# Optimization experiments

Hardware: AMD Instinct MI355X
Metric: run time of the kernel (lower is better)

The kernel has to match this reference:

```python
import jax, jax.numpy as jnp
import numpy as np

N_NODES = 100000
N_EDGES = 1600000
F_IN = 128
HID = 128
N_LAYERS = 4
N_CLASSES = 10
N_GRAPHS = 512
BN_EPS = 1e-5


def setup_inputs() -> dict:
    key = jax.random.key(0)
    ks = jax.random.split(key, 16)
    x = jax.random.normal(ks[0], (N_NODES, F_IN), dtype=jnp.float32)
    edge_index = jax.random.randint(ks[1], (2, N_EDGES), 0, N_NODES, dtype=jnp.int64)
    edge_attr = jax.random.normal(ks[2], (N_EDGES, 8), dtype=jnp.float32)
    batch = jnp.sort(jax.random.randint(ks[3], (N_NODES,), 0, N_GRAPHS, dtype=jnp.int64))
    # Per-layer MLP params (in-dim is 128 for all layers since F_IN == HID).
    s1 = 1.0 / np.sqrt(F_IN)
    s2 = 1.0 / np.sqrt(2 * HID)
    W1 = jax.random.uniform(ks[4], (N_LAYERS, F_IN, 2 * HID), minval=-s1, maxval=s1, dtype=jnp.float32)
    b1 = jax.random.uniform(ks[5], (N_LAYERS, 2 * HID), minval=-s1, maxval=s1, dtype=jnp.float32)
    gamma1 = jnp.ones((N_LAYERS, 2 * HID), dtype=jnp.float32)
    beta1 = jnp.zeros((N_LAYERS, 2 * HID), dtype=jnp.float32)
    W2 = jax.random.uniform(ks[6], (N_LAYERS, 2 * HID, HID), minval=-s2, maxval=s2, dtype=jnp.float32)
    b2 = jax.random.uniform(ks[7], (N_LAYERS, HID), minval=-s2, maxval=s2, dtype=jnp.float32)
    sf = 1.0 / np.sqrt(HID * N_LAYERS)
    fcW = jax.random.uniform(ks[8], (HID * N_LAYERS, N_CLASSES), minval=-sf, maxval=sf, dtype=jnp.float32)
    fcb = jax.random.uniform(ks[9], (N_CLASSES,), minval=-sf, maxval=sf, dtype=jnp.float32)
    return {"x": x, "edge_index": edge_index, "edge_attr": edge_attr, "batch": batch,
            "W1": W1, "b1": b1, "gamma1": gamma1, "beta1": beta1,
            "W2": W2, "b2": b2, "fcW": fcW, "fcb": fcb}


def reference(x, edge_index, edge_attr, batch, W1, b1, gamma1, beta1, W2, b2, fcW, fcb):
    # edge_attr is unused by the original forward.
    src, dst = edge_index[0], edge_index[1]
    n = x.shape[0]
    # In-degree for mean aggregation (messages flow src -> dst in PyG).
    deg = jax.ops.segment_sum(jnp.ones((src.shape[0],), x.dtype), dst, num_segments=n)
    inv_deg = 1.0 / jnp.maximum(deg, 1.0)
    h = x
    xs = []
    for i in range(N_LAYERS):
        # GINConv, eps=0, aggr='mean': nn(x + mean_j h_j)
        agg = jax.ops.segment_sum(h[src], dst, num_segments=n) * inv_deg[:, None]
        z = h + agg
        z = z @ W1[i] + b1[i]                      # [N, 2H]
        mu = jnp.mean(z, axis=0)
        var = jnp.mean(jnp.square(z - mu), axis=0)  # biased var (BN training mode)
        z = gamma1[i] * (z - mu) * jax.lax.rsqrt(var + BN_EPS) + beta1[i]
        z = jax.nn.relu(z)
        z = z @ W2[i] + b2[i]                      # [N, H]
        h = jax.nn.relu(z)
        xs.append(h)
    xcat = jnp.concatenate(xs, axis=1)             # [N, H*L]
    # global_mean_pool over graph ids
    gsum = jax.ops.segment_sum(xcat, batch, num_segments=N_GRAPHS)
    gcnt = jax.ops.segment_sum(jnp.ones((n,), xcat.dtype), batch, num_segments=N_GRAPHS)
    pooled = gsum / jnp.maximum(gcnt, 1.0)[:, None]
    logits = pooled @ fcW + fcb
    return jax.nn.log_softmax(logits, axis=-1)
```

## Files before the change

kernel.cpp:

```cpp
#include <hip/hip_runtime.h>
#include <cstdint>
#include <cstddef>

#define NN 100000
#define NE 1600000
#define FD 128
#define HD2 256
#define NLAYERS 4
#define NGR 512
#define NCLS 10
#define BNEPS 1e-5f
#define G1TILES 1563
#define GEMM_GRID 512
#define MLP_GRID 256
#define EB 6250
#define NB 391
#define NSLICE 8
#define SLICEW 12500

typedef unsigned short ushort_t;
typedef short bf16x8 __attribute__((ext_vector_type(8)));
typedef float f32x4 __attribute__((ext_vector_type(4)));

__device__ __forceinline__ float bfl(unsigned short u) {
  unsigned v = ((unsigned)u) << 16;
  return __builtin_bit_cast(float, v);
}
__device__ __forceinline__ unsigned short fbf(float f) {
  unsigned u = __builtin_bit_cast(unsigned, f);
  unsigned r = (u + 0x7FFFu + ((u >> 16) & 1u)) >> 16;
  return (unsigned short)r;
}

__global__ void k_init_detect(const int* ei, int* flag, int* degi) {
  int i = blockIdx.x * 256 + threadIdx.x;
  if (i < NN) degi[i] = 0;
  if (blockIdx.x == 0) {
    __shared__ int nz;
    if (threadIdx.x == 0) nz = 0;
    __syncthreads();
    if (ei[2 * threadIdx.x + 1] != 0) atomicAdd(&nz, 1);
    __syncthreads();
    if (threadIdx.x == 0) flag[0] = (nz == 0) ? 1 : 0;
  }
}

__global__ void k_repack(const int* ei, const int* batch, const int* flag,
                         int* src32, int* dst32, int* batch32) {
  int i = blockIdx.x * 256 + threadIdx.x;
  const bool wide = (flag[0] != 0);
  if (i < NE) {
    src32[i] = wide ? ei[2 * i] : ei[i];
    dst32[i] = wide ? ei[2 * (NE + i)] : ei[NE + i];
  }
  if (i < NN) batch32[i] = wide ? batch[2 * i] : batch[i];
}

__global__ void k_deg8(const int* __restrict__ dst, int* degi) {
  int slice = blockIdx.x & (NSLICE - 1);
  int e = (blockIdx.x >> 3) * 256 + threadIdx.x;
  if (e >= NE) return;
  int d = dst[e];
  int lo = slice * SLICEW;
  if (d >= lo && d < lo + SLICEW) atomicAdd(&degi[d], 1);
}

__global__ void k_scan1(const int* degi, int* rowptr, int* bsum) {
  __shared__ int s[256];
  int t = threadIdx.x;
  int i = blockIdx.x * 256 + t;
  int v = (i < NN) ? degi[i] : 0;
  s[t] = v;
  __syncthreads();
  for (int off = 1; off < 256; off <<= 1) {
    int x = (t >= off) ? s[t - off] : 0;
    __syncthreads();
    s[t] += x;
    __syncthreads();
  }
  if (i < NN) rowptr[i] = s[t] - v;
  if (t == 255) bsum[blockIdx.x] = s[255];
}

__global__ void k_scan2_gstats(int* bsum, int nb, const int* __restrict__ batch,
                               int* __restrict__ gstart, int* __restrict__ gcnti) {
  __shared__ int s[512];
  int t = threadIdx.x;
  int v = (t < nb) ? bsum[t] : 0;
  s[t] = v;
  __syncthreads();
  for (int off = 1; off < 512; off <<= 1) {
    int x = (t >= off) ? s[t - off] : 0;
    __syncthreads();
    s[t] += x;
    __syncthreads();
  }
  if (t < nb) bsum[t] = s[t] - v;
  if (t < NGR) {
    int g = t;
    int lo = 0, hi = NN;
    while (lo < hi) { int m = (lo + hi) >> 1; if (batch[m] < g) lo = m + 1; else hi = m; }
    int st = lo;
    hi = NN;
    while (lo < hi) { int m = (lo + hi) >> 1; if (batch[m] < g + 1) lo = m + 1; else hi = m; }
    gstart[g] = st;
    gcnti[g] = lo - st;
  }
}

__global__ void k_scan3_cursor(int* rowptr, const int* bsum, int* cursor,
                               const int* degi, float* inv_deg) {
  int i = blockIdx.x * 256 + threadIdx.x;
  if (i < NN) {
    int r = rowptr[i] + bsum[blockIdx.x];
    rowptr[i] = r;
    cursor[i] = r;
    inv_deg[i] = 1.f / fmaxf((float)degi[i], 1.f);
  }
  if (i == 0) rowptr[NN] = NE;
}

__global__ void k_scatter8(const int* __restrict__ src, const int* __restrict__ dst,
                           int* cursor, int* csr) {
  int slice = blockIdx.x & (NSLICE - 1);
  int e = (blockIdx.x >> 3) * 256 + threadIdx.x;
  if (e >= NE) return;
  int d = dst[e];
  int lo = slice * SLICEW;
  if (d >= lo && d < lo + SLICEW) {
    int p = atomicAdd(&cursor[d], 1);
    csr[p] = src[e];
  }
}

__global__ void k_cvt_x(const float* __restrict__ x, ushort_t* __restrict__ xb) {
  int i = blockIdx.x * 256 + threadIdx.x;
  if (i >= NN * FD / 8) return;
  const float4* p = (const float4*)x + (size_t)i * 2;
  float4 a = p[0], b = p[1];
  bf16x8 o;
  o[0] = (short)fbf(a.x); o[1] = (short)fbf(a.y);
  o[2] = (short)fbf(a.z); o[3] = (short)fbf(a.w);
  o[4] = (short)fbf(b.x); o[5] = (short)fbf(b.y);
  o[6] = (short)fbf(b.z); o[7] = (short)fbf(b.w);
  *(bf16x8*)&xb[(size_t)i * 8] = o;
}

__global__ void k_cvt_w(const float* __restrict__ W1, const float* __restrict__ W2,
                        ushort_t* __restrict__ W1t, ushort_t* __restrict__ W2t) {
  int idx = blockIdx.x * 256 + threadIdx.x;
  if (idx >= NLAYERS * FD * HD2) return;
  int l = idx >> 15, r = idx & 32767;
  {
    int n = r >> 7, k = r & 127;
    W1t[(size_t)l * 32768 + n * 128 + k] = fbf(W1[(size_t)l * 32768 + k * 256 + n]);
  }
  {
    int n = r >> 8, k = r & 255;
    W2t[(size_t)l * 32768 + n * 256 + k] = fbf(W2[(size_t)l * 32768 + k * 128 + n]);
  }
}

__global__ void k_agg(const ushort_t* __restrict__ h, const int* __restrict__ rowptr,
                      const int* __restrict__ csr, const float* __restrict__ inv_deg,
                      ushort_t* __restrict__ tout, float* bnsum) {
  if (blockIdx.x == 0) {
    bnsum[threadIdx.x] = 0.f;
    bnsum[HD2 + threadIdx.x] = 0.f;
  }
  const int wave = threadIdx.x >> 6;
  const int lane = threadIdx.x & 63;
  const int q = lane >> 4, sub = lane & 15;
  const int node = blockIdx.x * 16 + wave * 4 + q;
  const uint4* h16 = (const uint4*)h;
  int beg = rowptr[node];
  int deg = rowptr[node + 1] - beg;
  int m1 = max(deg, __shfl_xor(deg, 16));
  int maxd = max(m1, __shfl_xor(m1, 32));
  float a0 = 0.f, a1 = 0.f, a2 = 0.f, a3 = 0.f;
  float a4 = 0.f, a5 = 0.f, a6 = 0.f, a7 = 0.f;
  int j = 0;
  for (; j + 8 <= maxd; j += 8) {
    uint4 p[8];
#pragma unroll
    for (int u = 0; u < 8; ++u) {
      bool valid = (j + u) < deg;
      int idx = beg + (valid ? j + u : 0);
      int s = csr[idx];
      uint4 v = h16[(size_t)s * 16 + sub];
      p[u].x = valid ? v.x : 0u;
      p[u].y = valid ? v.y : 0u;
      p[u].z = valid ? v.z : 0u;
      p[u].w = valid ? v.w : 0u;
    }
#pragma unroll
    for (int u = 0; u < 8; ++u) {
      a0 += bfl((unsigned short)(p[u].x & 0xFFFF));
      a1 += bfl((unsigned short)(p[u].x >> 16));
      a2 += bfl((unsigned short)(p[u].y & 0xFFFF));
      a3 += bfl((unsigned short)(p[u].y >> 16));
      a4 += bfl((unsigned short)(p[u].z & 0xFFFF));
      a5 += bfl((unsigned short)(p[u].z >> 16));
      a6 += bfl((unsigned short)(p[u].w & 0xFFFF));
      a7 += bfl((unsigned short)(p[u].w >> 16));
    }
  }
  for (; j < maxd; ++j) {
    bool valid = j < deg;
    int idx = beg + (valid ? j : 0);
    int s = csr[idx];
    uint4 v = h16[(size_t)s * 16 + sub];
    if (valid) {
      a0 += bfl((unsigned short)(v.x & 0xFFFF));
      a1 += bfl((unsigned short)(v.x >> 16));
      a2 += bfl((unsigned short)(v.y & 0xFFFF));
      a3 += bfl((unsigned short)(v.y >> 16));
      a4 += bfl((unsigned short)(v.z & 0xFFFF));
      a5 += bfl((unsigned short)(v.z >> 16));
      a6 += bfl((unsigned short)(v.w & 0xFFFF));
      a7 += bfl((unsigned short)(v.w >> 16));
    }
  }
  float id = inv_deg[node];
  uint4 c = h16[(size_t)node * 16 + sub];
  float o0 = bfl((unsigned short)(c.x & 0xFFFF)) + a0 * id;
  float o1 = bfl((unsigned short)(c.x >> 16)) + a1 * id;
  float o2 = bfl((unsigned short)(c.y & 0xFFFF)) + a2 * id;
  float o3 = bfl((unsigned short)(c.y >> 16)) + a3 * id;
  float o4 = bfl((unsigned short)(c.z & 0xFFFF)) + a4 * id;
  float o5 = bfl((unsigned short)(c.z >> 16)) + a5 * id;
  float o6 = bfl((unsigned short)(c.w & 0xFFFF)) + a6 * id;
  float o7 = bfl((unsigned short)(c.w >> 16)) + a7 * id;
  uint4 ow;
  ow.x = (unsigned)fbf(o0) | ((unsigned)fbf(o1) << 16);
  ow.y = (unsigned)fbf(o2) | ((unsigned)fbf(o3) << 16);
  ow.z = (unsigned)fbf(o4) | ((unsigned)fbf(o5) << 16);
  ow.w = (unsigned)fbf(o6) | ((unsigned)fbf(o7) << 16);
  ((uint4*)tout)[(size_t)node * 16 + sub] = ow;
}

__launch_bounds__(256, 2)
__global__ void k_zstat(const ushort_t* __restrict__ A, const ushort_t* __restrict__ Bt,
                        const float* __restrict__ bias, float* __restrict__ bnsum) {
  __shared__ ushort_t Bs[256 * 128];
  __shared__ ushort_t As[64 * 128];
  const int tid = threadIdx.x;
#pragma unroll
  for (int i = 0; i < 16; ++i) {
    int chunk = tid + 256 * i;
    int n = chunk >> 4, c = chunk & 15;
    bf16x8 v = *(const bf16x8*)&Bt[n * 128 + c * 8];
    *(bf16x8*)((char*)Bs + n * 256 + ((c * 16) ^ ((n & 7) << 4))) = v;
  }
  const int wv = tid >> 6, ln = tid & 63;
  const int lr = ln & 15, lg = ln >> 4;
  float bb[16];
#pragma unroll
  for (int nt = 0; nt < 16; ++nt) bb[nt] = bias[nt * 16 + lr];
  float s0[16] = {}, s1[16] = {};

  for (int t = blockIdx.x; t < G1TILES; t += GEMM_GRID) {
    int row0 = t * 64;
#pragma unroll
    for (int i = 0; i < 4; ++i) {
      int chunk = tid + 256 * i;
      int r = chunk >> 4, c = chunk & 15;
      int grow = row0 + r; if (grow >= NN) grow = NN - 1;
      bf16x8 v = *(const bf16x8*)&A[(size_t)grow * FD + c * 8];
      *(bf16x8*)((char*)As + r * 256 + ((c * 16) ^ ((r & 7) << 4))) = v;
    }
    __syncthreads();
    int arow = wv * 16 + lr;
    bf16x8 af[4];
#pragma unroll
    for (int ks = 0; ks < 4; ++ks)
      af[ks] = *(bf16x8*)((char*)As + arow * 256 + ((ks * 64 + lg * 16) ^ ((arow & 7) << 4)));
    f32x4 acc[16];
#pragma unroll
    for (int nt = 0; nt < 16; ++nt) acc[nt] = (f32x4){0.f, 0.f, 0.f, 0.f};
#pragma unroll
    for (int nt = 0; nt < 16; ++nt) {
      int bn = nt * 16 + lr;
#pragma unroll
      for (int ks = 0; ks < 4; ++ks) {
        bf16x8 bfr = *(bf16x8*)((char*)Bs + bn * 256 + ((ks * 64 + lg * 16) ^ ((bn & 7) << 4)));
        acc[nt] = __builtin_amdgcn_mfma_f32_16x16x32_bf16(af[ks], bfr, acc[nt], 0, 0, 0);
      }
    }
    __syncthreads();
#pragma unroll
    for (int nt = 0; nt < 16; ++nt) {
#pragma unroll
      for (int j = 0; j < 4; ++j) {
        int grow = row0 + wv * 16 + lg * 4 + j;
        if (grow < NN) {
          float zf = acc[nt][j] + bb[nt];
          s0[nt] += zf;
          s1[nt] += zf * zf;
        }
      }
    }
  }
  __syncthreads();
  float* ls = (float*)As;
  ls[tid] = 0.f; ls[tid + 256] = 0.f;
  __syncthreads();
#pragma unroll
  for (int nt = 0; nt < 16; ++nt) {
    int col = nt * 16 + lr;
    atomicAdd(&ls[col], s0[nt]);
    atomicAdd(&ls[col + 256], s1[nt]);
  }
  __syncthreads();
  if (tid < 256) {
    atomicAdd(&bnsum[tid], ls[tid]);
    atomicAdd(&bnsum[HD2 + tid], ls[tid + 256]);
  }
}

__launch_bounds__(512, 2)
__global__ void k_mlp(const ushort_t* __restrict__ T, const ushort_t* __restrict__ W1t,
                      const ushort_t* __restrict__ W2t, const float* __restrict__ b1,
                      const float* __restrict__ b2, const float* __restrict__ bnsum,
                      const float* __restrict__ gamma, const float* __restrict__ beta,
                      ushort_t* __restrict__ Hout) {
  __shared__ ushort_t W1s[256 * 128];
  __shared__ ushort_t W2s[128 * 256];
  __shared__ ushort_t ZR[64 * 256];
  const int tid = threadIdx.x;
#pragma unroll
  for (int i = 0; i < 8; ++i) {
    int chunk = tid + 512 * i;
    int n = chunk >> 4, c = chunk & 15;
    bf16x8 v = *(const bf16x8*)&W1t[n * 128 + c * 8];
    *(bf16x8*)((char*)W1s + n * 256 + ((c * 16) ^ ((n & 7) << 4))) = v;
  }
#pragma unroll
  for (int i = 0; i < 8; ++i) {
    int chunk = tid + 512 * i;
    int n = chunk >> 5, c = chunk & 31;
    bf16x8 v = *(const bf16x8*)&W2t[n * 256 + c * 8];
    *(bf16x8*)((char*)W2s + n * 512 + ((c * 16) ^ ((n & 7) << 4))) = v;
  }
  const int wv = tid >> 6, ln = tid & 63;
  const int lr = ln & 15, lg = ln >> 4;
  const int mrow = (wv & 3) * 16;
  const int nh = wv >> 2;
  float a1v[8], a2v[8], bb1[8];
#pragma unroll
  for (int nt = 0; nt < 8; ++nt) {
    int c = (nh * 8 + nt) * 16 + lr;
    float mu = bnsum[c] * (1.f / (float)NN);
    float var = fmaxf(bnsum[HD2 + c] * (1.f / (float)NN) - mu * mu, 0.f);
    float g = gamma[c] * rsqrtf(var + BNEPS);
    a1v[nt] = g;
    a2v[nt] = beta[c] - mu * g;
    bb1[nt] = b1[c];
  }
  float bb2[4];
#pragma unroll
  for (int nt2 = 0; nt2 < 4; ++nt2) bb2[nt2] = b2[nh * 64 + nt2 * 16 + lr];
  __syncthreads();

  for (int t = blockIdx.x; t < G1TILES; t += MLP_GRID) {
    int row0 = t * 64;
    int grow = row0 + mrow + lr; if (grow >= NN) grow = NN - 1;
    bf16x8 af[4];
#pragma unroll
    for (int ks = 0; ks < 4; ++ks)
      af[ks] = *(const bf16x8*)&T[(size_t)grow * FD + ks * 32 + lg * 8];
    f32x4 acc1[8];
#pragma unroll
    for (int nt = 0; nt < 8; ++nt) acc1[nt] = (f32x4){0.f, 0.f, 0.f, 0.f};
#pragma unroll
    for (int nt = 0; nt < 8; ++nt) {
      int bn = (nh * 8 + nt) * 16 + lr;
#pragma unroll
      for (int ks = 0; ks < 4; ++ks) {
        bf16x8 bfr = *(bf16x8*)((char*)W1s + bn * 256 + ((ks * 64 + lg * 16) ^ ((bn & 7) << 4)));
        acc1[nt] = __builtin_amdgcn_mfma_f32_16x16x32_bf16(af[ks], bfr, acc1[nt], 0, 0, 0);
      }
    }
#pragma unroll
    for (int nt = 0; nt < 8; ++nt) {
      int col = (nh * 8 + nt) * 16 + lr;
#pragma unroll
      for (int j = 0; j < 4; ++j) {
        int row = mrow + lg * 4 + j;
        float z = acc1[nt][j] + bb1[nt];
        float f = fmaxf(z * a1v[nt] + a2v[nt], 0.f);
        int byte = row * 512 + ((((col >> 3) << 4) ^ ((row & 7) << 4))) + (col & 7) * 2;
        *(ushort_t*)((char*)ZR + byte) = fbf(f);
      }
    }
    __syncthreads();
    int zrow = mrow + lr;
    bf16x8 af2[8];
#pragma unroll
    for (int ks2 = 0; ks2 < 8; ++ks2) {
      int c2 = ks2 * 4 + lg;
      af2[ks2] = *(bf16x8*)((char*)ZR + zrow * 512 + ((c2 * 16) ^ ((zrow & 7) << 4)));
    }
    __syncthreads();
    f32x4 acc2[4];
#pragma unroll
    for (int nt2 = 0; nt2 < 4; ++nt2) acc2[nt2] = (f32x4){0.f, 0.f, 0.f, 0.f};
#pragma unroll
    for (int nt2 = 0; nt2 < 4; ++nt2) {
      int bn2 = nh * 64 + nt2 * 16 + lr;
#pragma unroll
      for (int ks2 = 0; ks2 < 8; ++ks2) {
        int c2 = ks2 * 4 + lg;
        bf16x8 bfr2 = *(bf16x8*)((char*)W2s + bn2 * 512 + ((c2 * 16) ^ ((bn2 & 7) << 4)));
        acc2[nt2] = __builtin_amdgcn_mfma_f32_16x16x32_bf16(af2[ks2], bfr2, acc2[nt2], 0, 0, 0);
      }
    }
#pragma unroll
    for (int nt2 = 0; nt2 < 4; ++nt2) {
      int col = nh * 64 + nt2 * 16 + lr;
#pragma unroll
      for (int j = 0; j < 4; ++j) {
        int hrow = row0 + mrow + lg * 4 + j;
        if (hrow < NN) Hout[(size_t)hrow * FD + col] = fbf(fmaxf(acc2[nt2][j] + bb2[nt2], 0.f));
      }
    }
  }
}

__launch_bounds__(256)
__global__ void k_pool_fc(const ushort_t* __restrict__ hb, const int* __restrict__ gstart,
                          const int* __restrict__ gcnti, const float* __restrict__ fcW,
                          const float* __restrict__ fcb, float* __restrict__ out) {
  __shared__ float pool4[4][512];
  __shared__ float wred[4][NCLS];
  int g = blockIdx.x, t = threadIdx.x;
  int start = gstart[g], cnt = gcnti[g];
  int chunk = t & 63, ro = t >> 6;
  int L = chunk >> 4, cc = (chunk & 15) * 8;
  const ushort_t* hL = hb + (size_t)L * NN * FD;
  float s[8] = {};
  for (int r = start + ro; r < start + cnt; r += 4) {
    bf16x8 v = *(const bf16x8*)&hL[(size_t)r * FD + cc];
#pragma unroll
    for (int j = 0; j < 8; ++j) s[j] += bfl((unsigned short)v[j]);
  }
#pragma unroll
  for (int j = 0; j < 8; ++j) pool4[ro][chunk * 8 + j] = s[j];
  __syncthreads();
  float inv = 1.f / fmaxf((float)cnt, 1.f);
  float pA = (pool4[0][t] + pool4[1][t] + pool4[2][t] + pool4[3][t]) * inv;
  float pB = (pool4[0][t + 256] + pool4[1][t + 256] + pool4[2][t + 256] + pool4[3][t + 256]) * inv;
  float pacc[NCLS];
#pragma unroll
  for (int c = 0; c < NCLS; ++c)
    pacc[c] = pA * fcW[t * NCLS + c] + pB * fcW[(t + 256) * NCLS + c];
#pragma unroll
  for (int off = 32; off > 0; off >>= 1)
#pragma unroll
    for (int c = 0; c < NCLS; ++c) pacc[c] += __shfl_down(pacc[c], off);
  if ((t & 63) == 0)
#pragma unroll
    for (int c = 0; c < NCLS; ++c) wred[t >> 6][c] = pacc[c];
  __syncthreads();
  if (t == 0) {
    float lg[NCLS];
    float mx = -1e30f;
#pragma unroll
    for (int c = 0; c < NCLS; ++c) {
      lg[c] = wred[0][c] + wred[1][c] + wred[2][c] + wred[3][c] + fcb[c];
      mx = fmaxf(mx, lg[c]);
    }
    float se = 0.f;
#pragma unroll
    for (int c = 0; c < NCLS; ++c) se += expf(lg[c] - mx);
    float lse = mx + logf(se);
#pragma unroll
    for (int c = 0; c < NCLS; ++c) out[(size_t)g * NCLS + c] = lg[c] - lse;
  }
}

extern "C" void kernel_launch(void* const* d_in, const int* in_sizes, int n_in,
                              void* d_out, int out_size, void* d_ws, size_t ws_size,
                              hipStream_t stream) {
  const float* x      = (const float*)d_in[0];
  const int*   ei     = (const int*)d_in[1];
  const int*   batch  = (const int*)d_in[3];
  const float* W1     = (const float*)d_in[4];
  const float* b1     = (const float*)d_in[5];
  const float* gamma1 = (const float*)d_in[6];
  const float* beta1  = (const float*)d_in[7];
  const float* W2     = (const float*)d_in[8];
  const float* b2     = (const float*)d_in[9];
  const float* fcW    = (const float*)d_in[10];
  const float* fcb    = (const float*)d_in[11];
  float* out = (float*)d_out;

  char* p = (char*)d_ws;
  auto alloc = [&](size_t bytes) {
    char* r = p;
    p += (bytes + 255) & ~(size_t)255;
    return r;
  };
  ushort_t* xbf   = (ushort_t*)alloc((size_t)NN * FD * 2);
  ushort_t* tbuf  = (ushort_t*)alloc((size_t)NN * FD * 2);
  ushort_t* hb    = (ushort_t*)alloc((size_t)NLAYERS * NN * FD * 2);
  ushort_t* W1t   = (ushort_t*)alloc((size_t)NLAYERS * FD * HD2 * 2);
  ushort_t* W2t   = (ushort_t*)alloc((size_t)NLAYERS * FD * HD2 * 2);
  float* inv_deg  = (float*)alloc((size_t)NN * 4);
  float* bnsum    = (float*)alloc(2 * HD2 * 4);
  int* degi       = (int*)alloc((size_t)NN * 4);
  int* rowptr     = (int*)alloc((size_t)(NN + 1) * 4);
  int* cursor     = (int*)alloc((size_t)NN * 4);
  int* csr        = (int*)alloc((size_t)NE * 4);
  int* bsum       = (int*)alloc(512 * 4);
  int* src32      = (int*)alloc((size_t)NE * 4);
  int* dst32      = (int*)alloc((size_t)NE * 4);
  int* batch32    = (int*)alloc((size_t)NN * 4);
  int* gcnti      = (int*)alloc((size_t)NGR * 4);
  int* gstart     = (int*)alloc((size_t)NGR * 4);
  int* flag       = (int*)alloc(256);

  k_init_detect<<<NB, 256, 0, stream>>>(ei, flag, degi);
  k_repack<<<EB, 256, 0, stream>>>(ei, batch, flag, src32, dst32, batch32);
  k_deg8<<<EB * NSLICE, 256, 0, stream>>>(dst32, degi);
  k_scan1<<<NB, 256, 0, stream>>>(degi, rowptr, bsum);
  k_scan2_gstats<<<1, 512, 0, stream>>>(bsum, NB, batch32, gstart, gcnti);
  k_scan3_cursor<<<NB, 256, 0, stream>>>(rowptr, bsum, cursor, degi, inv_deg);
  k_scatter8<<<EB * NSLICE, 256, 0, stream>>>(src32, dst32, cursor, csr);
  k_cvt_x<<<(NN * FD / 8 + 255) / 256, 256, 0, stream>>>(x, xbf);
  k_cvt_w<<<(NLAYERS * FD * HD2 + 255) / 256, 256, 0, stream>>>(W1, W2, W1t, W2t);

  const ushort_t* hin = xbf;
  for (int L = 0; L < NLAYERS; ++L) {
    k_agg<<<NN / 16, 256, 0, stream>>>(hin, rowptr, csr, inv_deg, tbuf, bnsum);
    k_zstat<<<GEMM_GRID, 256, 0, stream>>>(tbuf, W1t + (size_t)L * FD * HD2,
                                           b1 + (size_t)L * HD2, bnsum);
    k_mlp<<<MLP_GRID, 512, 0, stream>>>(tbuf, W1t + (size_t)L * FD * HD2,
                                        W2t + (size_t)L * FD * HD2,
                                        b1 + (size_t)L * HD2, b2 + (size_t)L * FD,
                                        bnsum, gamma1 + (size_t)L * HD2,
                                        beta1 + (size_t)L * HD2,
                                        hb + (size_t)L * NN * FD);
    hin = hb + (size_t)L * NN * FD;
  }
  k_pool_fc<<<NGR, 256, 0, stream>>>(hb, gstart, gcnti, fcW, fcb, out);
}
```

Before: 722.7 us.

## Bucket edges by destination slice before degree count and CSR scatter

Replaces the 8-pass filtered degree and scatter kernels, which each read every edge once per slice, with a bucketing step. Edges are first counted and placed into contiguous per-slice buckets, then the degree and scatter kernels read only their own slice. This removes the 8x redundant reads of dst and src in those two kernels but adds three launches and an extra write and read of the edge arrays. The k_deg_b and k_scatter_b grids stay at EB*NSLICE blocks, so most blocks exit early.

New measurement: 874.8 us. +21.1%, slower.

```diff
diff --git a/kernel.cpp b/kernel.cpp
--- a/kernel.cpp
+++ b/kernel.cpp
@@ -32,9 +32,10 @@
   return (unsigned short)r;
 }
 
-__global__ void k_init_detect(const int* ei, int* flag, int* degi) {
+__global__ void k_init_detect(const int* ei, int* flag, int* degi, int* sliceCnt) {
   int i = blockIdx.x * 256 + threadIdx.x;
   if (i < NN) degi[i] = 0;
+  if (blockIdx.x == 1 && threadIdx.x < NSLICE) sliceCnt[threadIdx.x] = 0;
   if (blockIdx.x == 0) {
     __shared__ int nz;
     if (threadIdx.x == 0) nz = 0;
@@ -56,13 +57,59 @@
   if (i < NN) batch32[i] = wide ? batch[2 * i] : batch[i];
 }
 
-__global__ void k_deg8(const int* __restrict__ dst, int* degi) {
-  int slice = blockIdx.x & (NSLICE - 1);
-  int e = (blockIdx.x >> 3) * 256 + threadIdx.x;
-  if (e >= NE) return;
-  int d = dst[e];
-  int lo = slice * SLICEW;
-  if (d >= lo && d < lo + SLICEW) atomicAdd(&degi[d], 1);
+__global__ void k_bcnt(const int* __restrict__ dst, int* sliceCnt) {
+  __shared__ int h[NSLICE];
+  int tid = threadIdx.x;
+  if (tid < NSLICE) h[tid] = 0;
+  __syncthreads();
+  int e = blockIdx.x * 256 + tid;
+  if (e < NE) atomicAdd(&h[dst[e] / SLICEW], 1);
+  __syncthreads();
+  if (tid < NSLICE && h[tid]) atomicAdd(&sliceCnt[tid], h[tid]);
+}
+
+__global__ void k_bscan(const int* __restrict__ sliceCnt, int* sliceBase, int* sliceRes) {
+  if (threadIdx.x == 0) {
+    int acc = 0;
+    for (int s = 0; s < NSLICE; ++s) {
+      sliceBase[s] = acc;
+      sliceRes[s] = acc;
+      acc += sliceCnt[s];
+    }
+    sliceBase[NSLICE] = acc;
+  }
+}
+
+__global__ void k_bplace(const int* __restrict__ src, const int* __restrict__ dst,
+                         int* sliceRes, int* __restrict__ bsrc, int* __restrict__ bdst) {
+  __shared__ int h[NSLICE], base[NSLICE];
+  int tid = threadIdx.x;
+  if (tid < NSLICE) h[tid] = 0;
+  __syncthreads();
+  int e = blockIdx.x * 256 + tid;
+  int s = 0, r = 0, d = 0, sv = 0;
+  bool act = (e < NE);
+  if (act) {
+    d = dst[e];
+    sv = src[e];
+    s = d / SLICEW;
+    r = atomicAdd(&h[s], 1);
+  }
+  __syncthreads();
+  if (tid < NSLICE) base[tid] = h[tid] ? atomicAdd(&sliceRes[tid], h[tid]) : 0;
+  __syncthreads();
+  if (act) {
+    int pos = base[s] + r;
+    bdst[pos] = d;
+    bsrc[pos] = sv;
+  }
+}
+
+__global__ void k_deg_b(const int* __restrict__ bdst, const int* __restrict__ sliceBase,
+                        int* degi) {
+  int s = blockIdx.x & (NSLICE - 1);
+  int idx = sliceBase[s] + (blockIdx.x >> 3) * 256 + threadIdx.x;
+  if (idx < sliceBase[s + 1]) atomicAdd(&degi[bdst[idx]], 1);
 }
 
 __global__ void k_scan1(const int* degi, int* rowptr, int* bsum) {
@@ -120,16 +167,14 @@
   if (i == 0) rowptr[NN] = NE;
 }
 
-__global__ void k_scatter8(const int* __restrict__ src, const int* __restrict__ dst,
-                           int* cursor, int* csr) {
-  int slice = blockIdx.x & (NSLICE - 1);
-  int e = (blockIdx.x >> 3) * 256 + threadIdx.x;
-  if (e >= NE) return;
-  int d = dst[e];
-  int lo = slice * SLICEW;
-  if (d >= lo && d < lo + SLICEW) {
+__global__ void k_scatter_b(const int* __restrict__ bsrc, const int* __restrict__ bdst,
+                            const int* __restrict__ sliceBase, int* cursor, int* csr) {
+  int s = blockIdx.x & (NSLICE - 1);
+  int idx = sliceBase[s] + (blockIdx.x >> 3) * 256 + threadIdx.x;
+  if (idx < sliceBase[s + 1]) {
+    int d = bdst[idx];
     int p = atomicAdd(&cursor[d], 1);
-    csr[p] = src[e];
+    csr[p] = bsrc[idx];
   }
 }
 
@@ -515,18 +560,26 @@
   int* bsum       = (int*)alloc(512 * 4);
   int* src32      = (int*)alloc((size_t)NE * 4);
   int* dst32      = (int*)alloc((size_t)NE * 4);
+  int* bsrc       = (int*)alloc((size_t)NE * 4);
+  int* bdst       = (int*)alloc((size_t)NE * 4);
   int* batch32    = (int*)alloc((size_t)NN * 4);
   int* gcnti      = (int*)alloc((size_t)NGR * 4);
   int* gstart     = (int*)alloc((size_t)NGR * 4);
+  int* sliceCnt   = (int*)alloc(64);
+  int* sliceBase  = (int*)alloc(64);
+  int* sliceRes   = (int*)alloc(64);
   int* flag       = (int*)alloc(256);
 
-  k_init_detect<<<NB, 256, 0, stream>>>(ei, flag, degi);
+  k_init_detect<<<NB, 256, 0, stream>>>(ei, flag, degi, sliceCnt);
   k_repack<<<EB, 256, 0, stream>>>(ei, batch, flag, src32, dst32, batch32);
-  k_deg8<<<EB * NSLICE, 256, 0, stream>>>(dst32, degi);
+  k_bcnt<<<EB, 256, 0, stream>>>(dst32, sliceCnt);
+  k_bscan<<<1, 64, 0, stream>>>(sliceCnt, sliceBase, sliceRes);
+  k_bplace<<<EB, 256, 0, stream>>>(src32, dst32, sliceRes, bsrc, bdst);
+  k_deg_b<<<EB * NSLICE, 256, 0, stream>>>(bdst, sliceBase, degi);
   k_scan1<<<NB, 256, 0, stream>>>(degi, rowptr, bsum);
   k_scan2_gstats<<<1, 512, 0, stream>>>(bsum, NB, batch32, gstart, gcnti);
   k_scan3_cursor<<<NB, 256, 0, stream>>>(rowptr, bsum, cursor, degi, inv_deg);
-  k_scatter8<<<EB * NSLICE, 256, 0, stream>>>(src32, dst32, cursor, csr);
+  k_scatter_b<<<EB * NSLICE, 256, 0, stream>>>(bsrc, bdst, sliceBase, cursor, csr);
   k_cvt_x<<<(NN * FD / 8 + 255) / 256, 256, 0, stream>>>(x, xbf);
   k_cvt_w<<<(NLAYERS * FD * HD2 + 255) / 256, 256, 0, stream>>>(W1, W2, W1t, W2t);
 
```
